# Kernel tuning notes

Hardware: AMD Instinct MI355X
Metric: run time of the kernel (lower is better)

Reference implementation:

```python
import jax, jax.numpy as jnp
import numpy as np

N = 50000
IN_DIM = 256
HID = 64
HEADS = 4
OUT_DIM = 40
E = 800000
NEG_SLOPE = 0.2


def setup_inputs() -> dict:
    key = jax.random.key(0)
    ks = jax.random.split(key, 12)
    x = jax.random.normal(ks[0], (N, IN_DIM), dtype=jnp.float32)
    edge_index = jax.random.randint(ks[1], (2, E), 0, N, dtype=jnp.int64)
    s = 0.05
    W1 = jax.random.normal(ks[2], (IN_DIM, HEADS * HID), dtype=jnp.float32) * s
    att_src1 = jax.random.normal(ks[3], (HEADS, HID), dtype=jnp.float32) * s
    att_dst1 = jax.random.normal(ks[4], (HEADS, HID), dtype=jnp.float32) * s
    b1 = jnp.zeros((HEADS * HID,), dtype=jnp.float32)
    W2 = jax.random.normal(ks[5], (HEADS * HID, OUT_DIM), dtype=jnp.float32) * s
    att_src2 = jax.random.normal(ks[6], (1, OUT_DIM), dtype=jnp.float32) * s
    att_dst2 = jax.random.normal(ks[7], (1, OUT_DIM), dtype=jnp.float32) * s
    b2 = jnp.zeros((OUT_DIM,), dtype=jnp.float32)
    return {"x": x, "edge_index": edge_index, "W1": W1, "att_src1": att_src1,
            "att_dst1": att_dst1, "b1": b1, "W2": W2, "att_src2": att_src2,
            "att_dst2": att_dst2, "b2": b2}


def _gat_conv(x, src, dst, W, a_src, a_dst, b, heads, out_ch, concat):
    n = x.shape[0]
    h = (x @ W).reshape(n, heads, out_ch)              # [N,H,C]
    alpha_s = jnp.einsum('nhc,hc->nh', h, a_src)       # [N,H]
    alpha_d = jnp.einsum('nhc,hc->nh', h, a_dst)
    e = jax.nn.leaky_relu(alpha_s[src] + alpha_d[dst], NEG_SLOPE)  # [E,H]
    # segment softmax over destination neighborhoods
    m = jax.ops.segment_max(e, dst, num_segments=n)    # [N,H]
    ex = jnp.exp(e - m[dst])
    denom = jax.ops.segment_sum(ex, dst, num_segments=n)
    alpha = ex / (denom[dst] + 1e-16)                  # [E,H]
    out = jax.ops.segment_sum(h[src] * alpha[:, :, None], dst, num_segments=n)  # [N,H,C]
    out = out.reshape(n, heads * out_ch) if concat else out.mean(axis=1)
    return out + b


def reference(x, edge_index, W1, att_src1, att_dst1, b1, W2, att_src2, att_dst2, b2):
    # PyG GATConv adds self-loops by default
    loops = jnp.arange(N, dtype=edge_index.dtype)
    src = jnp.concatenate([edge_index[0], loops])
    dst = jnp.concatenate([edge_index[1], loops])
    h = _gat_conv(x, src, dst, W1, att_src1, att_dst1, b1, HEADS, HID, True)
    h = jax.nn.elu(h)
    h = _gat_conv(h, src, dst, W2, att_src2, att_dst2, b2, 1, OUT_DIM, False)
    return jax.nn.log_softmax(h, axis=1)
```

## Files before the change

kernel.cpp:

```cpp
#include <hip/hip_runtime.h>
#include <hip/hip_bf16.h>
#include <math.h>

#define NNODES 50000
#define M_PAD  50048
#define IN_DIM 256
#define HID 64
#define HEADS 4
#define OUT_DIM 40
#define NEDGES 800000
#define ETOT (NEDGES + NNODES)
#define NEG_SLOPE 0.2f
#define MAXDEG 64
#define SCAT_CH 416
#define PREP_BLKS (307 + SCAT_CH * 8)

typedef __attribute__((ext_vector_type(8))) short bf16x8;
typedef __attribute__((ext_vector_type(4))) float f32x4;
typedef __attribute__((ext_vector_type(2))) float f32x2;
typedef unsigned char uchar;

__device__ __forceinline__ ushort f2bf(float f) {
    uint u = __float_as_uint(f);
    u += 0x7FFF + ((u >> 16) & 1);
    return (ushort)(u >> 16);
}
__device__ __forceinline__ uint fkey(float f) {
    uint u = __float_as_uint(f);
    return (u & 0x80000000u) ? ~u : (u | 0x80000000u);
}
__device__ __forceinline__ float fdec(uint k) {
    return (k & 0x80000000u) ? __uint_as_float(k & 0x7fffffffu) : __uint_as_float(~k);
}
__device__ __forceinline__ float wave_reduce_max(float v) {
    #pragma unroll
    for (int off = 32; off > 0; off >>= 1) v = fmaxf(v, __shfl_xor(v, off));
    return v;
}
__device__ __forceinline__ float wave_reduce_sum(float v) {
    #pragma unroll
    for (int off = 32; off > 0; off >>= 1) v += __shfl_xor(v, off);
    return v;
}
__device__ __forceinline__ uchar f2fp8(float v) {
    return (uchar)(__builtin_amdgcn_cvt_pk_fp8_f32(v, v, 0, false) & 0xFF);
}
__device__ __forceinline__ void accum8f8(f32x2* acc2, uint2 hv, float wgt) {
    f32x2 wv = {wgt, wgt};
    f32x2 p;
    p = __builtin_amdgcn_cvt_pk_f32_fp8(hv.x, false); acc2[0] += p * wv;
    p = __builtin_amdgcn_cvt_pk_f32_fp8(hv.x, true);  acc2[1] += p * wv;
    p = __builtin_amdgcn_cvt_pk_f32_fp8(hv.y, false); acc2[2] += p * wv;
    p = __builtin_amdgcn_cvt_pk_f32_fp8(hv.y, true);  acc2[3] += p * wv;
}
__device__ __forceinline__ float lrw(float e, float mm) {
    return __expf(fmaxf(e, NEG_SLOPE * e) - mm);
}
__device__ __forceinline__ uint dpart(int d) {
    return ((uint)d * 10737u) >> 26;
}

__global__ void prep_kernel(const float* __restrict__ W1, const float* __restrict__ W2,
                            const float* __restrict__ a2s, const float* __restrict__ a2d,
                            const int* __restrict__ ei,
                            ushort* __restrict__ W1t, ushort* __restrict__ W2tb,
                            float* __restrict__ wa_s, float* __restrict__ wa_d,
                            int* __restrict__ counts, int* __restrict__ col) {
    int b = blockIdx.x, t = threadIdx.x;
    if (b >= 307) {
        int b2 = b - 307;
        uint part = (uint)(b2 & 7);
        int chunk = b2 >> 3;
        int base = chunk * 2048 + t * 8;
        if (base >= ETOT) return;
        int s[8], d[8];
        if (base + 8 <= NEDGES) {
            int4 sa = *reinterpret_cast<const int4*>(ei + base);
            int4 sb = *reinterpret_cast<const int4*>(ei + base + 4);
            int4 da = *reinterpret_cast<const int4*>(ei + NEDGES + base);
            int4 db = *reinterpret_cast<const int4*>(ei + NEDGES + base + 4);
            s[0] = sa.x; s[1] = sa.y; s[2] = sa.z; s[3] = sa.w;
            s[4] = sb.x; s[5] = sb.y; s[6] = sb.z; s[7] = sb.w;
            d[0] = da.x; d[1] = da.y; d[2] = da.z; d[3] = da.w;
            d[4] = db.x; d[5] = db.y; d[6] = db.z; d[7] = db.w;
        } else {
            #pragma unroll
            for (int k = 0; k < 8; k++) {
                int idx = base + k;
                if (idx < NEDGES) { s[k] = ei[idx]; d[k] = ei[NEDGES + idx]; }
                else if (idx < ETOT) { s[k] = idx - NEDGES; d[k] = s[k]; }
                else { s[k] = 0; d[k] = -1; }
            }
        }
        #pragma unroll
        for (int k = 0; k < 8; k++) {
            if (d[k] >= 0 && dpart(d[k]) == part) {
                int pos = atomicAdd(&counts[d[k]], 1);
                if (pos < MAXDEG) col[d[k] * MAXDEG + pos] = s[k];
            }
        }
        return;
    }
    if (b < 256) {
        W1t[b * 256 + t] = f2bf(W1[t * 256 + b]);
    } else if (b < 306) {
        int idx = (b - 256) * 256 + t;
        if (idx < 48 * 264) {
            int n = idx / 264, k = idx % 264;
            W2tb[idx] = (n < OUT_DIM && k < 256) ? f2bf(W2[k * OUT_DIM + n]) : (ushort)0;
        }
    } else {
        float ss = 0.f, sd = 0.f;
        #pragma unroll 8
        for (int c = 0; c < OUT_DIM; c++) {
            float wv = W2[t * OUT_DIM + c];
            ss += wv * a2s[c];
            sd += wv * a2d[c];
        }
        wa_s[t] = ss;
        wa_d[t] = sd;
    }
}

__global__ __launch_bounds__(256) void gemm1_fused(const float* __restrict__ x,
                                                   const ushort* __restrict__ W1t,
                                                   const float* __restrict__ asrc,
                                                   const float* __restrict__ adst,
                                                   uchar* __restrict__ h1f8,
                                                   float* __restrict__ as1,
                                                   float* __restrict__ ad1,
                                                   uint* __restrict__ gb) {
    __shared__ ushort As[64 * 32];
    __shared__ ushort Bs[256 * 32];
    __shared__ uint smax[4];
    int t = threadIdx.x;
    int l = t & 63, wn = t >> 6;
    int m0 = blockIdx.x * 64;
    int lrow = l & 15, lks = l >> 4;
    int ks = lks ^ ((lrow >> 1) & 3);

    f32x4 acc[4][4];
    #pragma unroll
    for (int i = 0; i < 4; i++)
        #pragma unroll
        for (int j = 0; j < 4; j++) acc[i][j] = (f32x4){0.f, 0.f, 0.f, 0.f};

    for (int k0 = 0; k0 < 256; k0 += 32) {
        #pragma unroll
        for (int i = 0; i < 2; i++) {
            int idx = t + 256 * i;
            int row = idx >> 3, c4 = idx & 7;
            int grow = m0 + row;
            float4 v = make_float4(0.f, 0.f, 0.f, 0.f);
            if (grow < NNODES) v = *reinterpret_cast<const float4*>(x + (size_t)grow * 256 + k0 + c4 * 4);
            uint2 p;
            p.x = (uint)f2bf(v.x) | ((uint)f2bf(v.y) << 16);
            p.y = (uint)f2bf(v.z) | ((uint)f2bf(v.w) << 16);
            int slot = (c4 >> 1) ^ ((row >> 1) & 3);
            *reinterpret_cast<uint2*>(&As[row * 32 + slot * 8 + (c4 & 1) * 4]) = p;
        }
        #pragma unroll
        for (int i = 0; i < 4; i++) {
            int idx = t + 256 * i;
            int row = idx >> 2, skb = idx & 3;
            uint4 bv = *reinterpret_cast<const uint4*>(W1t + (size_t)row * 256 + k0 + skb * 8);
            int slot = skb ^ ((row >> 1) & 3);
            *reinterpret_cast<uint4*>(&Bs[row * 32 + slot * 8]) = bv;
        }
        __syncthreads();
        bf16x8 a_frag[4], b_frag[4];
        #pragma unroll
        for (int mf = 0; mf < 4; mf++)
            a_frag[mf] = *reinterpret_cast<const bf16x8*>(&As[(mf * 16 + lrow) * 32 + ks * 8]);
        #pragma unroll
        for (int nf = 0; nf < 4; nf++)
            b_frag[nf] = *reinterpret_cast<const bf16x8*>(&Bs[(wn * 64 + nf * 16 + lrow) * 32 + ks * 8]);
        #pragma unroll
        for (int mf = 0; mf < 4; mf++)
            #pragma unroll
            for (int nf = 0; nf < 4; nf++)
                acc[mf][nf] = __builtin_amdgcn_mfma_f32_16x16x32_bf16(a_frag[mf], b_frag[nf], acc[mf][nf], 0, 0, 0);
        __syncthreads();
    }

    #pragma unroll
    for (int mf = 0; mf < 4; mf++)
        #pragma unroll
        for (int nf = 0; nf < 4; nf++) {
            int col_ = wn * 64 + nf * 16 + lrow;
            #pragma unroll
            for (int r = 0; r < 4; r++) {
                int row = m0 + mf * 16 + lks * 4 + r;
                h1f8[(size_t)row * 256 + col_] = f2fp8(acc[mf][nf][r]);
            }
        }

    float a_s[4], a_d[4];
    #pragma unroll
    for (int nf = 0; nf < 4; nf++) {
        a_s[nf] = asrc[wn * 64 + nf * 16 + lrow];
        a_d[nf] = adst[wn * 64 + nf * 16 + lrow];
    }
    float ps[4][4], pd[4][4];
    #pragma unroll
    for (int mf = 0; mf < 4; mf++)
        #pragma unroll
        for (int r = 0; r < 4; r++) {
            float s = 0.f, d = 0.f;
            #pragma unroll
            for (int nf = 0; nf < 4; nf++) {
                s += acc[mf][nf][r] * a_s[nf];
                d += acc[mf][nf][r] * a_d[nf];
            }
            ps[mf][r] = s; pd[mf][r] = d;
        }
    #pragma unroll
    for (int off = 1; off < 16; off <<= 1)
        #pragma unroll
        for (int mf = 0; mf < 4; mf++)
            #pragma unroll
            for (int r = 0; r < 4; r++) {
                ps[mf][r] += __shfl_xor(ps[mf][r], off);
                pd[mf][r] += __shfl_xor(pd[mf][r], off);
            }
    if (lrow == 0) {
        #pragma unroll
        for (int mf = 0; mf < 4; mf++)
            #pragma unroll
            for (int r = 0; r < 4; r++) {
                int row = m0 + mf * 16 + lks * 4 + r;
                if (row < NNODES) {
                    as1[row * 4 + wn] = ps[mf][r];
                    ad1[row * 4 + wn] = pd[mf][r];
                }
            }
    }
    float vmax = -INFINITY;
    #pragma unroll
    for (int mf = 0; mf < 4; mf++)
        #pragma unroll
        for (int r = 0; r < 4; r++) {
            int row = m0 + mf * 16 + lks * 4 + r;
            if (row < NNODES) vmax = fmaxf(vmax, ps[mf][r]);
        }
    vmax = fmaxf(vmax, __shfl_xor(vmax, 16));
    vmax = fmaxf(vmax, __shfl_xor(vmax, 32));
    if (l == 0) smax[wn] = fkey(vmax);
    __syncthreads();
    if (t < 4) atomicMax(&gb[t], smax[t]);
}

__global__ __launch_bounds__(256) void agg1_kernel(const uchar* __restrict__ h1f8,
                                                   const float* __restrict__ as1,
                                                   const float* __restrict__ ad1,
                                                   const int* __restrict__ cnt,
                                                   const int* __restrict__ col,
                                                   const float* __restrict__ b1,
                                                   const uint* __restrict__ gb,
                                                   const float* __restrict__ wa_s,
                                                   const float* __restrict__ wa_d,
                                                   ushort* __restrict__ out1b,
                                                   float* __restrict__ as2,
                                                   float* __restrict__ ad2) {
    int tid = threadIdx.x;
    int lane = tid & 63, wid = tid >> 6;
    int n = blockIdx.x * 4 + wid;
    int j = lane & 31, half = lane >> 5;
    int myh = j >> 3, sub = j & 3;
    int bcast = lane & ~3;
    int deg = min(cnt[n], MAXDEG);
    const int* cp = col + n * MAXDEG;

    float adn = ad1[n * 4 + myh];
    float g = fdec(gb[myh]);
    float mt = g + adn;
    float mm = fmaxf(mt, NEG_SLOPE * mt);

    f32x2 acc2[4];
    #pragma unroll
    for (int k = 0; k < 4; k++) acc2[k] = (f32x2){0.f, 0.f};
    float ls = 0.f;
    uint jb = (uint)(j * 8);

    int done = 0;
    for (; done + 8 <= deg; done += 8) {
        const int* p = cp + done + half * 4;
        int4 ca = *reinterpret_cast<const int4*>(p);
        int sown = sub == 0 ? ca.x : sub == 1 ? ca.y : sub == 2 ? ca.z : ca.w;
        float q = as1[(uint)(sown * 4 + myh)];
        uint2 h0 = *reinterpret_cast<const uint2*>(h1f8 + (((uint)ca.x << 8) + jb));
        uint2 h1v = *reinterpret_cast<const uint2*>(h1f8 + (((uint)ca.y << 8) + jb));
        uint2 h2v = *reinterpret_cast<const uint2*>(h1f8 + (((uint)ca.z << 8) + jb));
        uint2 h3v = *reinterpret_cast<const uint2*>(h1f8 + (((uint)ca.w << 8) + jb));
        float wown = lrw(q + adn, mm);
        float w0 = __shfl(wown, bcast + 0);
        float w1 = __shfl(wown, bcast + 1);
        float w2 = __shfl(wown, bcast + 2);
        float w3 = __shfl(wown, bcast + 3);
        ls += (w0 + w1) + (w2 + w3);
        accum8f8(acc2, h0, w0);
        accum8f8(acc2, h1v, w1);
        accum8f8(acc2, h2v, w2);
        accum8f8(acc2, h3v, w3);
    }
    if (done < deg) {
        int base = done + half * 4;
        int4 ca = *reinterpret_cast<const int4*>(cp + base);
        int s0 = (base + 0 < deg) ? ca.x : 0;
        int s1 = (base + 1 < deg) ? ca.y : 0;
        int s2 = (base + 2 < deg) ? ca.z : 0;
        int s3 = (base + 3 < deg) ? ca.w : 0;
        int sown = sub == 0 ? s0 : sub == 1 ? s1 : sub == 2 ? s2 : s3;
        float q = as1[(uint)(sown * 4 + myh)];
        uint2 h0 = *reinterpret_cast<const uint2*>(h1f8 + (((uint)s0 << 8) + jb));
        uint2 h1v = *reinterpret_cast<const uint2*>(h1f8 + (((uint)s1 << 8) + jb));
        uint2 h2v = *reinterpret_cast<const uint2*>(h1f8 + (((uint)s2 << 8) + jb));
        uint2 h3v = *reinterpret_cast<const uint2*>(h1f8 + (((uint)s3 << 8) + jb));
        float wown = (base + sub < deg) ? lrw(q + adn, mm) : 0.f;
        float w0 = __shfl(wown, bcast + 0);
        float w1 = __shfl(wown, bcast + 1);
        float w2 = __shfl(wown, bcast + 2);
        float w3 = __shfl(wown, bcast + 3);
        ls += (w0 + w1) + (w2 + w3);
        accum8f8(acc2, h0, w0);
        accum8f8(acc2, h1v, w1);
        accum8f8(acc2, h2v, w2);
        accum8f8(acc2, h3v, w3);
    }
    #pragma unroll
    for (int k = 0; k < 4; k++) {
        acc2[k].x += __shfl_xor(acc2[k].x, 32);
        acc2[k].y += __shfl_xor(acc2[k].y, 32);
    }
    ls += __shfl_xor(ls, 32);

    float dinv = 1.f / (ls + 1e-16f);
    float4 bA = *reinterpret_cast<const float4*>(b1 + j * 8);
    float4 bB = *reinterpret_cast<const float4*>(b1 + j * 8 + 4);
    float4 wsA = *reinterpret_cast<const float4*>(wa_s + j * 8);
    float4 wsB = *reinterpret_cast<const float4*>(wa_s + j * 8 + 4);
    float4 wdA = *reinterpret_cast<const float4*>(wa_d + j * 8);
    float4 wdB = *reinterpret_cast<const float4*>(wa_d + j * 8 + 4);
    float o[8];
    o[0] = acc2[0].x * dinv + bA.x; o[1] = acc2[0].y * dinv + bA.y;
    o[2] = acc2[1].x * dinv + bA.z; o[3] = acc2[1].y * dinv + bA.w;
    o[4] = acc2[2].x * dinv + bB.x; o[5] = acc2[2].y * dinv + bB.y;
    o[6] = acc2[3].x * dinv + bB.z; o[7] = acc2[3].y * dinv + bB.w;
    #pragma unroll
    for (int e8 = 0; e8 < 8; e8++) o[e8] = o[e8] > 0.f ? o[e8] : (__expf(o[e8]) - 1.f);
    float dps = o[0] * wsA.x + o[1] * wsA.y + o[2] * wsA.z + o[3] * wsA.w
              + o[4] * wsB.x + o[5] * wsB.y + o[6] * wsB.z + o[7] * wsB.w;
    float dpd = o[0] * wdA.x + o[1] * wdA.y + o[2] * wdA.z + o[3] * wdA.w
              + o[4] * wdB.x + o[5] * wdB.y + o[6] * wdB.z + o[7] * wdB.w;
    #pragma unroll
    for (int off = 1; off < 32; off <<= 1) {
        dps += __shfl_xor(dps, off);
        dpd += __shfl_xor(dpd, off);
    }
    if (lane == 0) { as2[n] = dps; ad2[n] = dpd; }
    if (lane < 32) {
        uint4 pk;
        pk.x = (uint)f2bf(o[0]) | ((uint)f2bf(o[1]) << 16);
        pk.y = (uint)f2bf(o[2]) | ((uint)f2bf(o[3]) << 16);
        pk.z = (uint)f2bf(o[4]) | ((uint)f2bf(o[5]) << 16);
        pk.w = (uint)f2bf(o[6]) | ((uint)f2bf(o[7]) << 16);
        *reinterpret_cast<uint4*>(out1b + ((uint)n * 256 + (uint)j * 8)) = pk;
    }
}

__global__ __launch_bounds__(256) void gemm2_kernel(const ushort* __restrict__ Ag,
                                                    const ushort* __restrict__ Bg,
                                                    const float* __restrict__ as2,
                                                    uchar* __restrict__ h2f8,
                                                    uint* __restrict__ gb) {
    __shared__ ushort Bs[48 * 264];
    int t = threadIdx.x;
    int l = t & 63, w = t >> 6;
    int lrow = l & 15, lks = l >> 4;
    for (int idx = t; idx < 48 * 264 / 8; idx += 256)
        reinterpret_cast<uint4*>(Bs)[idx] = reinterpret_cast<const uint4*>(Bg)[idx];
    __syncthreads();

    int m0 = blockIdx.x * 64 + w * 16;
    f32x4 acc[3];
    #pragma unroll
    for (int nf = 0; nf < 3; nf++) acc[nf] = (f32x4){0.f, 0.f, 0.f, 0.f};

    #pragma unroll
    for (int k0 = 0; k0 < 256; k0 += 32) {
        bf16x8 af = *reinterpret_cast<const bf16x8*>(Ag + (size_t)(m0 + lrow) * 256 + k0 + lks * 8);
        #pragma unroll
        for (int nf = 0; nf < 3; nf++) {
            bf16x8 bf = *reinterpret_cast<const bf16x8*>(&Bs[(nf * 16 + lrow) * 264 + k0 + lks * 8]);
            acc[nf] = __builtin_amdgcn_mfma_f32_16x16x32_bf16(af, bf, acc[nf], 0, 0, 0);
        }
    }
    #pragma unroll
    for (int nf = 0; nf < 3; nf++) {
        int c = nf * 16 + lrow;
        if (c < OUT_DIM) {
            #pragma unroll
            for (int r = 0; r < 4; r++) {
                int row = m0 + lks * 4 + r;
                if (row < NNODES) h2f8[(size_t)row * OUT_DIM + c] = f2fp8(acc[nf][r]);
            }
        }
    }
    if (t < 64) {
        int row = blockIdx.x * 64 + t;
        float v = (row < NNODES) ? as2[row] : -INFINITY;
        v = wave_reduce_max(v);
        if (t == 0) atomicMax(&gb[4], fkey(v));
    }
}

__global__ __launch_bounds__(256) void agg2_kernel(const uchar* __restrict__ h2f8,
                                                   const float* __restrict__ as2,
                                                   const float* __restrict__ ad2,
                                                   const int* __restrict__ cnt,
                                                   const int* __restrict__ col,
                                                   const float* __restrict__ b2,
                                                   const uint* __restrict__ gb,
                                                   float* __restrict__ out) {
    int tid = threadIdx.x;
    int lane = tid & 63, wid = tid >> 6;
    int n = blockIdx.x * 4 + wid;
    int j = lane & 31, half = lane >> 5;
    int sub = j & 3;
    int bcast = lane & ~3;
    int deg = min(cnt[n], MAXDEG);
    const int* cp = col + n * MAXDEG;
    float adn = ad2[n];
    float g = fdec(gb[4]);
    float mt = g + adn;
    float mm = fmaxf(mt, NEG_SLOPE * mt);

    bool act = j < 20;
    uint jo = (uint)(j * 2);
    f32x2 a2 = {0.f, 0.f};
    float ls = 0.f;

    int done = 0;
    for (; done + 8 <= deg; done += 8) {
        const int* p = cp + done + half * 4;
        int4 ca = *reinterpret_cast<const int4*>(p);
        int sown = sub == 0 ? ca.x : sub == 1 ? ca.y : sub == 2 ? ca.z : ca.w;
        float q = as2[(uint)sown];
        uint v0 = 0, v1 = 0, v2 = 0, v3 = 0;
        if (act) {
            v0 = *reinterpret_cast<const ushort*>(h2f8 + ((uint)ca.x * 40 + jo));
            v1 = *reinterpret_cast<const ushort*>(h2f8 + ((uint)ca.y * 40 + jo));
            v2 = *reinterpret_cast<const ushort*>(h2f8 + ((uint)ca.z * 40 + jo));
            v3 = *reinterpret_cast<const ushort*>(h2f8 + ((uint)ca.w * 40 + jo));
        }
        float wown = lrw(q + adn, mm);
        float w0 = __shfl(wown, bcast + 0);
        float w1 = __shfl(wown, bcast + 1);
        float w2 = __shfl(wown, bcast + 2);
        float w3 = __shfl(wown, bcast + 3);
        ls += (w0 + w1) + (w2 + w3);
        a2 += __builtin_amdgcn_cvt_pk_f32_fp8(v0, false) * (f32x2){w0, w0};
        a2 += __builtin_amdgcn_cvt_pk_f32_fp8(v1, false) * (f32x2){w1, w1};
        a2 += __builtin_amdgcn_cvt_pk_f32_fp8(v2, false) * (f32x2){w2, w2};
        a2 += __builtin_amdgcn_cvt_pk_f32_fp8(v3, false) * (f32x2){w3, w3};
    }
    if (done < deg) {
        int base = done + half * 4;
        int4 ca = *reinterpret_cast<const int4*>(cp + base);
        int s0 = (base + 0 < deg) ? ca.x : 0;
        int s1 = (base + 1 < deg) ? ca.y : 0;
        int s2 = (base + 2 < deg) ? ca.z : 0;
        int s3 = (base + 3 < deg) ? ca.w : 0;
        int sown = sub == 0 ? s0 : sub == 1 ? s1 : sub == 2 ? s2 : s3;
        float q = as2[(uint)sown];
        uint v0 = 0, v1 = 0, v2 = 0, v3 = 0;
        if (act) {
            v0 = *reinterpret_cast<const ushort*>(h2f8 + ((uint)s0 * 40 + jo));
            v1 = *reinterpret_cast<const ushort*>(h2f8 + ((uint)s1 * 40 + jo));
            v2 = *reinterpret_cast<const ushort*>(h2f8 + ((uint)s2 * 40 + jo));
            v3 = *reinterpret_cast<const ushort*>(h2f8 + ((uint)s3 * 40 + jo));
        }
        float wown = (base + sub < deg) ? lrw(q + adn, mm) : 0.f;
        float w0 = __shfl(wown, bcast + 0);
        float w1 = __shfl(wown, bcast + 1);
        float w2 = __shfl(wown, bcast + 2);
        float w3 = __shfl(wown, bcast + 3);
        ls += (w0 + w1) + (w2 + w3);
        a2 += __builtin_amdgcn_cvt_pk_f32_fp8(v0, false) * (f32x2){w0, w0};
        a2 += __builtin_amdgcn_cvt_pk_f32_fp8(v1, false) * (f32x2){w1, w1};
        a2 += __builtin_amdgcn_cvt_pk_f32_fp8(v2, false) * (f32x2){w2, w2};
        a2 += __builtin_amdgcn_cvt_pk_f32_fp8(v3, false) * (f32x2){w3, w3};
    }
    a2.x += __shfl_xor(a2.x, 32);
    a2.y += __shfl_xor(a2.y, 32);
    ls += __shfl_xor(ls, 32);

    bool lead = lane < 20;
    float v0 = -INFINITY, v1 = -INFINITY;
    if (lead) {
        float2 bb = *reinterpret_cast<const float2*>(b2 + 2 * j);
        float dinv = 1.f / (ls + 1e-16f);
        v0 = a2.x * dinv + bb.x;
        v1 = a2.y * dinv + bb.y;
    }
    float mx = wave_reduce_max(fmaxf(v0, v1));
    float es = lead ? (__expf(v0 - mx) + __expf(v1 - mx)) : 0.f;
    float ssum = wave_reduce_sum(es);
    float lg = __logf(ssum);
    if (lead) {
        float2 o2 = make_float2(v0 - mx - lg, v1 - mx - lg);
        *reinterpret_cast<float2*>(out + (size_t)n * OUT_DIM + 2 * j) = o2;
    }
}

extern "C" void kernel_launch(void* const* d_in, const int* in_sizes, int n_in,
                              void* d_out, int out_size, void* d_ws, size_t ws_size,
                              hipStream_t stream) {
    const float* x        = (const float*)d_in[0];
    const int*   ei       = (const int*)d_in[1];
    const float* W1       = (const float*)d_in[2];
    const float* att_src1 = (const float*)d_in[3];
    const float* att_dst1 = (const float*)d_in[4];
    const float* b1       = (const float*)d_in[5];
    const float* W2       = (const float*)d_in[6];
    const float* att_src2 = (const float*)d_in[7];
    const float* att_dst2 = (const float*)d_in[8];
    const float* b2       = (const float*)d_in[9];
    float* out = (float*)d_out;

    char* ws = (char*)d_ws;
    auto alloc = [&](size_t bytes) {
        char* p = ws;
        ws += (bytes + 255) & ~(size_t)255;
        return p;
    };
    uchar*  h1f8   = (uchar*)alloc((size_t)M_PAD * 256);
    ushort* out1b  = (ushort*)alloc((size_t)M_PAD * 256 * 2);
    ushort* W1t    = (ushort*)alloc((size_t)256 * 256 * 2);
    ushort* W2tb   = (ushort*)alloc((size_t)48 * 264 * 2);
    uchar*  h2f8   = (uchar*)alloc((size_t)M_PAD * OUT_DIM);
    float*  as1    = (float*)alloc((size_t)NNODES * 4 * 4);
    float*  ad1    = (float*)alloc((size_t)NNODES * 4 * 4);
    float*  as2    = (float*)alloc((size_t)NNODES * 4);
    float*  ad2    = (float*)alloc((size_t)NNODES * 4);
    float*  wa_s   = (float*)alloc((size_t)256 * 4);
    float*  wa_d   = (float*)alloc((size_t)256 * 4);
    int*    counts = (int*)alloc((size_t)(NNODES + 8) * 4);
    uint*   gmaxb  = (uint*)(counts + NNODES);
    int*    col    = (int*)alloc((size_t)NNODES * MAXDEG * 4);
    if ((size_t)(ws - (char*)d_ws) > ws_size) return;

    hipMemsetAsync(counts, 0, (size_t)(NNODES + 8) * 4, stream);

    prep_kernel<<<PREP_BLKS, 256, 0, stream>>>(W1, W2, att_src2, att_dst2, ei,
                                               W1t, W2tb, wa_s, wa_d, counts, col);

    gemm1_fused<<<M_PAD / 64, 256, 0, stream>>>(x, W1t, att_src1, att_dst1,
                                                h1f8, as1, ad1, gmaxb);
    agg1_kernel<<<NNODES / 4, 256, 0, stream>>>(h1f8, as1, ad1, counts, col, b1, gmaxb,
                                                wa_s, wa_d, out1b, as2, ad2);
    gemm2_kernel<<<M_PAD / 64, 256, 0, stream>>>(out1b, W2tb, as2, h2f8, gmaxb);
    agg2_kernel<<<NNODES / 4, 256, 0, stream>>>(h2f8, as2, ad2, counts, col, b2, gmaxb, out);
}
```

Before: 170.8 us.

## Stage full A row-block in LDS once and read W1 fragments directly from global

The GEMM1 kernel now loads the whole 64x256 bf16 activation tile into shared memory up front with an XOR swizzle, instead of staging A and B in 32-wide K slices. The B (W1t) fragments are read straight from global memory/cache per wave, which removes the per-iteration syncthreads and the B shared-memory staging. This cuts barriers and LDS traffic in the K loop, at the cost of larger LDS use (32KB) and uncoalesced-ish global reads for W1 that rely on L2/L1 hits.

```diff
diff --git a/kernel.cpp b/kernel.cpp
--- a/kernel.cpp
+++ b/kernel.cpp
@@ -130,14 +130,29 @@
                                                    float* __restrict__ as1,
                                                    float* __restrict__ ad1,
                                                    uint* __restrict__ gb) {
-    __shared__ ushort As[64 * 32];
-    __shared__ ushort Bs[256 * 32];
+    __shared__ ushort As[64 * 256];
     __shared__ uint smax[4];
     int t = threadIdx.x;
     int l = t & 63, wn = t >> 6;
     int m0 = blockIdx.x * 64;
     int lrow = l & 15, lks = l >> 4;
-    int ks = lks ^ ((lrow >> 1) & 3);
+
+    #pragma unroll 4
+    for (int i = 0; i < 16; i++) {
+        int idx = t + i * 256;
+        int row = idx >> 6;
+        int c4 = idx & 63;
+        int grow = m0 + row;
+        float4 v = make_float4(0.f, 0.f, 0.f, 0.f);
+        if (grow < NNODES) v = *reinterpret_cast<const float4*>(x + (size_t)grow * 256 + c4 * 4);
+        uint2 p;
+        p.x = (uint)f2bf(v.x) | ((uint)f2bf(v.y) << 16);
+        p.y = (uint)f2bf(v.z) | ((uint)f2bf(v.w) << 16);
+        int cc = c4 >> 1, half = c4 & 1;
+        int slot = cc ^ (row & 7);
+        *reinterpret_cast<uint2*>(&As[row * 256 + (slot << 3) + (half << 2)]) = p;
+    }
+    __syncthreads();
 
     f32x4 acc[4][4];
     #pragma unroll
@@ -145,44 +160,28 @@
         #pragma unroll
         for (int j = 0; j < 4; j++) acc[i][j] = (f32x4){0.f, 0.f, 0.f, 0.f};
 
+    #pragma unroll 2
     for (int k0 = 0; k0 < 256; k0 += 32) {
-        #pragma unroll
-        for (int i = 0; i < 2; i++) {
-            int idx = t + 256 * i;
-            int row = idx >> 3, c4 = idx & 7;
-            int grow = m0 + row;
-            float4 v = make_float4(0.f, 0.f, 0.f, 0.f);
-            if (grow < NNODES) v = *reinterpret_cast<const float4*>(x + (size_t)grow * 256 + k0 + c4 * 4);
-            uint2 p;
-            p.x = (uint)f2bf(v.x) | ((uint)f2bf(v.y) << 16);
-            p.y = (uint)f2bf(v.z) | ((uint)f2bf(v.w) << 16);
-            int slot = (c4 >> 1) ^ ((row >> 1) & 3);
-            *reinterpret_cast<uint2*>(&As[row * 32 + slot * 8 + (c4 & 1) * 4]) = p;
-        }
-        #pragma unroll
-        for (int i = 0; i < 4; i++) {
-            int idx = t + 256 * i;
-            int row = idx >> 2, skb = idx & 3;
-            uint4 bv = *reinterpret_cast<const uint4*>(W1t + (size_t)row * 256 + k0 + skb * 8);
-            int slot = skb ^ ((row >> 1) & 3);
-            *reinterpret_cast<uint4*>(&Bs[row * 32 + slot * 8]) = bv;
-        }
-        __syncthreads();
-        bf16x8 a_frag[4], b_frag[4];
-        #pragma unroll
-        for (int mf = 0; mf < 4; mf++)
-            a_frag[mf] = *reinterpret_cast<const bf16x8*>(&As[(mf * 16 + lrow) * 32 + ks * 8]);
-        #pragma unroll
-        for (int nf = 0; nf < 4; nf++)
-            b_frag[nf] = *reinterpret_cast<const bf16x8*>(&Bs[(wn * 64 + nf * 16 + lrow) * 32 + ks * 8]);
+        bf16x8 b_frag[4], a_frag[4];
+        #pragma unroll
+        for (int nf = 0; nf < 4; nf++) {
+            int row = wn * 64 + nf * 16 + lrow;
+            b_frag[nf] = *reinterpret_cast<const bf16x8*>(W1t + (size_t)row * 256 + k0 + lks * 8);
+        }
+        int cc = (k0 >> 3) + lks;
+        #pragma unroll
+        for (int mf = 0; mf < 4; mf++) {
+            int row = mf * 16 + lrow;
+            a_frag[mf] = *reinterpret_cast<const bf16x8*>(&As[row * 256 + ((cc ^ (row & 7)) << 3)]);
+        }
         #pragma unroll
         for (int mf = 0; mf < 4; mf++)
             #pragma unroll
             for (int nf = 0; nf < 4; nf++)
                 acc[mf][nf] = __builtin_amdgcn_mfma_f32_16x16x32_bf16(a_frag[mf], b_frag[nf], acc[mf][nf], 0, 0, 0);
-        __syncthreads();
-    }
-
+    }
+
+    int lks4 = (l >> 4) * 4;
     #pragma unroll
     for (int mf = 0; mf < 4; mf++)
         #pragma unroll
@@ -190,7 +189,7 @@
             int col_ = wn * 64 + nf * 16 + lrow;
             #pragma unroll
             for (int r = 0; r < 4; r++) {
-                int row = m0 + mf * 16 + lks * 4 + r;
+                int row = m0 + mf * 16 + lks4 + r;
                 h1f8[(size_t)row * 256 + col_] = f2fp8(acc[mf][nf][r]);
             }
         }
@@ -228,7 +227,7 @@
         for (int mf = 0; mf < 4; mf++)
             #pragma unroll
             for (int r = 0; r < 4; r++) {
-                int row = m0 + mf * 16 + lks * 4 + r;
+                int row = m0 + mf * 16 + lks4 + r;
                 if (row < NNODES) {
                     as1[row * 4 + wn] = ps[mf][r];
                     ad1[row * 4 + wn] = pd[mf][r];
@@ -240,7 +239,7 @@
     for (int mf = 0; mf < 4; mf++)
         #pragma unroll
         for (int r = 0; r < 4; r++) {
-            int row = m0 + mf * 16 + lks * 4 + r;
+            int row = m0 + mf * 16 + lks4 + r;
             if (row < NNODES) vmax = fmaxf(vmax, ps[mf][r]);
         }
     vmax = fmaxf(vmax, __shfl_xor(vmax, 16));
```

Measured after the change: 176.3 us. 3.3% more time.
